# Performance work log

Measured on AMD Instinct MI355X. Metric: run time of the kernel, lower is better.

## Reference

```python
import jax, jax.numpy as jnp
import numpy as np

EPS = 1e-5

def _layer_norm(x, gamma, beta):
    m = jnp.mean(x, axis=-1, keepdims=True)
    v = jnp.mean(jnp.square(x - m), axis=-1, keepdims=True)
    return (x - m) * jax.lax.rsqrt(v + EPS) * gamma + beta

def setup_inputs() -> dict:
    key = jax.random.key(0)
    ks = jax.random.split(key, 6)
    B, D, H = 4096, 1024, 1024
    s = 1.0 / np.sqrt(H)
    return {
        "inputs": jax.random.normal(ks[0], (B, D), jnp.float32),
        "hx": jax.random.normal(ks[1], (B, H), jnp.float32),
        "cx": jax.random.normal(ks[2], (B, H), jnp.float32),
        "w_ih": jax.random.uniform(ks[3], (4 * H, D), jnp.float32, -s, s),
        "w_hh": jax.random.uniform(ks[4], (4 * H, H), jnp.float32, -s, s),
        "b_hh": jax.random.uniform(ks[5], (4 * H,), jnp.float32, -s, s),
        "g_ih": jnp.ones((4 * H,), jnp.float32),
        "beta_ih": jnp.zeros((4 * H,), jnp.float32),
        "g_hh": jnp.ones((4 * H,), jnp.float32),
        "beta_hh": jnp.zeros((4 * H,), jnp.float32),
        "g_ho": jnp.ones((H,), jnp.float32),
        "beta_ho": jnp.zeros((H,), jnp.float32),
    }

def reference(inputs, hx, cx, w_ih, w_hh, b_hh, g_ih, beta_ih, g_hh, beta_hh, g_ho, beta_ho):
    # i2h: [B, 4H] (no input bias used in original forward)
    i2h = inputs @ w_ih.T
    h2h = hx @ w_hh.T + b_hh
    gates = _layer_norm(i2h, g_ih, beta_ih) + _layer_norm(h2h, g_hh, beta_hh)
    i, f, o, g = jnp.split(gates, 4, axis=1)  # torch chunk order: i, f, o, g
    cy = jax.nn.sigmoid(f) * cx + jax.nn.sigmoid(i) * jnp.tanh(g)
    hy = jax.nn.sigmoid(o) * _layer_norm(jnp.tanh(cy), g_ho, beta_ho)
    # Dropout(0.1) is identity in eval / deterministic reference
    return hy, cy
```

## Files before the change

### kernel.cpp

```cpp
#include <hip/hip_runtime.h>
#include <hip/hip_bf16.h>
#include <stdint.h>

typedef __attribute__((ext_vector_type(8))) short bf16x8;
typedef __attribute__((ext_vector_type(4))) float f32x4;

#define LN_EPS 1e-5f

__device__ inline unsigned f2bf(float f) {
    unsigned u = __builtin_bit_cast(unsigned, f);
    u += 0x7fffu + ((u >> 16) & 1u);
    return u >> 16;
}
__device__ inline float bf2f(unsigned u) {
    return __builtin_bit_cast(float, u << 16);
}
__device__ inline float sigf(float x) {
    return 1.0f / (1.0f + __expf(-x));
}
__device__ inline float tanh_fast(float x) {
    return __builtin_fmaf(2.0f, 1.0f / (1.0f + __expf(-2.0f * x)), -1.0f);
}
__device__ inline float wred(float v) {
#pragma unroll
    for (int o = 32; o > 0; o >>= 1) v += __shfl_xor(v, o);
    return v;
}
__device__ inline void gload_lds16(const void* g, void* l) {
    __builtin_amdgcn_global_load_lds(
        (const __attribute__((address_space(1))) void*)g,
        (__attribute__((address_space(3))) void*)l, 16, 0, 0);
}

__global__ __launch_bounds__(256) void cast_all(
    const float4* __restrict__ s0, ushort4* __restrict__ d0, int n0,
    const float4* __restrict__ s1, ushort4* __restrict__ d1, int n1,
    const float4* __restrict__ s2, ushort4* __restrict__ d2, int n2,
    const float4* __restrict__ s3, ushort4* __restrict__ d3, int n3)
{
    int j = blockIdx.x * blockDim.x + threadIdx.x;
    const float4* s; ushort4* d;
    if (j < n0) { s = s0; d = d0; }
    else {
        j -= n0;
        if (j < n1) { s = s1; d = d1; }
        else {
            j -= n1;
            if (j < n2) { s = s2; d = d2; }
            else {
                j -= n2;
                if (j >= n3) return;
                s = s3; d = d3;
            }
        }
    }
    float4 v = s[j];
    ushort4 o;
    o.x = (unsigned short)f2bf(v.x); o.y = (unsigned short)f2bf(v.y);
    o.z = (unsigned short)f2bf(v.z); o.w = (unsigned short)f2bf(v.w);
    d[j] = o;
}

#define GNT 32

__global__ __launch_bounds__(512) void gemm8p(
    const short* __restrict__ Aa, const short* __restrict__ Ba, unsigned short* __restrict__ Ca,
    const short* __restrict__ Ab, const short* __restrict__ Bb, unsigned short* __restrict__ Cb,
    const float* __restrict__ Bias,
    float2* __restrict__ P,
    int N, int K)
{
    __shared__ __attribute__((aligned(16))) short lds[65536];
    short* ldsA = lds;
    short* ldsB = lds + 32768;

    const int gx  = gridDim.x;
    const int gxy = gx * gridDim.y;
    int bid = (blockIdx.z * gridDim.y + blockIdx.y) * gx + blockIdx.x;
    const int cpx = (gxy * gridDim.z) >> 3;
    int swz = (bid & 7) * cpx + (bid >> 3);
    const int z  = swz / gxy;
    const int r2 = swz - z * gxy;
    const int by = r2 / gx;
    const int bx = r2 - by * gx;

    const short* __restrict__ A = z ? Ab : Aa;
    const short* __restrict__ B = z ? Bb : Ba;
    unsigned short* __restrict__ C = z ? Cb : Ca;
    const int brow = by * 256, bcol = bx * 256;

    const int t    = threadIdx.x;
    const int lane = t & 63, w = t >> 6;
    const int wr = w >> 2, wc = w & 3;
    const int lr = lane & 15, kc = lane >> 4;

    const int ci0 = t, ci1 = t + 512;
    const int r0 = ci0 >> 2, l0 = (ci0 & 3) ^ ((r0 >> 1) & 3);
    const int r1 = ci1 >> 2, l1 = (ci1 & 3) ^ ((r1 >> 1) & 3);
    const int gA0 = (brow + r0) * K + l0 * 8;
    const int gA1 = (brow + r1) * K + l1 * 8;
    const int gB0 = (bcol + r0) * K + l0 * 8;
    const int gB1 = (bcol + r1) * K + l1 * 8;
    const int d0 = ci0 * 8, d1 = ci1 * 8;

#define STAGE_A(u) { const int so_ = ((u) & 3) * 8192; \
    gload_lds16(A + gA0 + (u) * 32, ldsA + so_ + d0);  \
    gload_lds16(A + gA1 + (u) * 32, ldsA + so_ + d1); }
#define STAGE_B(u) { const int so_ = ((u) & 3) * 8192; \
    gload_lds16(B + gB0 + (u) * 32, ldsB + so_ + d0);  \
    gload_lds16(B + gB1 + (u) * 32, ldsB + so_ + d1); }

    int offW[8], offX[4];
#pragma unroll
    for (int f = 0; f < 8; ++f) {
        int r = wr * 128 + f * 16 + lr;
        offW[f] = r * 32 + ((kc ^ ((r >> 1) & 3)) * 8);
    }
#pragma unroll
    for (int n = 0; n < 4; ++n) {
        int r = wc * 64 + n * 16 + lr;
        offX[n] = r * 32 + ((kc ^ ((r >> 1) & 3)) * 8);
    }

    f32x4 acc[8][4];
#pragma unroll
    for (int i = 0; i < 8; ++i)
#pragma unroll
        for (int j = 0; j < 4; ++j)
            acc[i][j] = (f32x4){0.f, 0.f, 0.f, 0.f};

    STAGE_A(0); STAGE_B(0); STAGE_A(1); STAGE_B(1); STAGE_A(2);
    asm volatile("s_waitcnt vmcnt(6)" ::: "memory");
    __builtin_amdgcn_s_barrier();

#pragma unroll 4
    for (int T = 0; T < GNT; ++T) {
        const int so = (T & 3) * 8192;
        bf16x8 w0, w1, w2, w3, x0, x1, x2, x3;

        w0 = *(const bf16x8*)&ldsB[so + offW[0]];
        w1 = *(const bf16x8*)&ldsB[so + offW[1]];
        w2 = *(const bf16x8*)&ldsB[so + offW[2]];
        w3 = *(const bf16x8*)&ldsB[so + offW[3]];
        x0 = *(const bf16x8*)&ldsA[so + offX[0]];
        x1 = *(const bf16x8*)&ldsA[so + offX[1]];
        x2 = *(const bf16x8*)&ldsA[so + offX[2]];
        x3 = *(const bf16x8*)&ldsA[so + offX[3]];
        if (T + 2 < GNT) STAGE_B(T + 2);
        __builtin_amdgcn_s_barrier();
        asm volatile("s_waitcnt lgkmcnt(0)" ::: "memory");
        __builtin_amdgcn_sched_barrier(0);
        __builtin_amdgcn_s_setprio(1);
        acc[0][0] = __builtin_amdgcn_mfma_f32_16x16x32_bf16(w0, x0, acc[0][0], 0, 0, 0);
        acc[0][1] = __builtin_amdgcn_mfma_f32_16x16x32_bf16(w0, x1, acc[0][1], 0, 0, 0);
        acc[0][2] = __builtin_amdgcn_mfma_f32_16x16x32_bf16(w0, x2, acc[0][2], 0, 0, 0);
        acc[0][3] = __builtin_amdgcn_mfma_f32_16x16x32_bf16(w0, x3, acc[0][3], 0, 0, 0);
        acc[1][0] = __builtin_amdgcn_mfma_f32_16x16x32_bf16(w1, x0, acc[1][0], 0, 0, 0);
        acc[1][1] = __builtin_amdgcn_mfma_f32_16x16x32_bf16(w1, x1, acc[1][1], 0, 0, 0);
        acc[1][2] = __builtin_amdgcn_mfma_f32_16x16x32_bf16(w1, x2, acc[1][2], 0, 0, 0);
        acc[1][3] = __builtin_amdgcn_mfma_f32_16x16x32_bf16(w1, x3, acc[1][3], 0, 0, 0);
        acc[2][0] = __builtin_amdgcn_mfma_f32_16x16x32_bf16(w2, x0, acc[2][0], 0, 0, 0);
        acc[2][1] = __builtin_amdgcn_mfma_f32_16x16x32_bf16(w2, x1, acc[2][1], 0, 0, 0);
        acc[2][2] = __builtin_amdgcn_mfma_f32_16x16x32_bf16(w2, x2, acc[2][2], 0, 0, 0);
        acc[2][3] = __builtin_amdgcn_mfma_f32_16x16x32_bf16(w2, x3, acc[2][3], 0, 0, 0);
        acc[3][0] = __builtin_amdgcn_mfma_f32_16x16x32_bf16(w3, x0, acc[3][0], 0, 0, 0);
        acc[3][1] = __builtin_amdgcn_mfma_f32_16x16x32_bf16(w3, x1, acc[3][1], 0, 0, 0);
        acc[3][2] = __builtin_amdgcn_mfma_f32_16x16x32_bf16(w3, x2, acc[3][2], 0, 0, 0);
        acc[3][3] = __builtin_amdgcn_mfma_f32_16x16x32_bf16(w3, x3, acc[3][3], 0, 0, 0);
        __builtin_amdgcn_s_setprio(0);
        __builtin_amdgcn_s_barrier();

        w0 = *(const bf16x8*)&ldsB[so + offW[4]];
        w1 = *(const bf16x8*)&ldsB[so + offW[5]];
        w2 = *(const bf16x8*)&ldsB[so + offW[6]];
        w3 = *(const bf16x8*)&ldsB[so + offW[7]];
        if (T + 3 < GNT) STAGE_A(T + 3);
        __builtin_amdgcn_s_barrier();
        asm volatile("s_waitcnt lgkmcnt(0)" ::: "memory");
        __builtin_amdgcn_sched_barrier(0);
        __builtin_amdgcn_s_setprio(1);
        acc[4][0] = __builtin_amdgcn_mfma_f32_16x16x32_bf16(w0, x0, acc[4][0], 0, 0, 0);
        acc[4][1] = __builtin_amdgcn_mfma_f32_16x16x32_bf16(w0, x1, acc[4][1], 0, 0, 0);
        acc[4][2] = __builtin_amdgcn_mfma_f32_16x16x32_bf16(w0, x2, acc[4][2], 0, 0, 0);
        acc[4][3] = __builtin_amdgcn_mfma_f32_16x16x32_bf16(w0, x3, acc[4][3], 0, 0, 0);
        acc[5][0] = __builtin_amdgcn_mfma_f32_16x16x32_bf16(w1, x0, acc[5][0], 0, 0, 0);
        acc[5][1] = __builtin_amdgcn_mfma_f32_16x16x32_bf16(w1, x1, acc[5][1], 0, 0, 0);
        acc[5][2] = __builtin_amdgcn_mfma_f32_16x16x32_bf16(w1, x2, acc[5][2], 0, 0, 0);
        acc[5][3] = __builtin_amdgcn_mfma_f32_16x16x32_bf16(w1, x3, acc[5][3], 0, 0, 0);
        acc[6][0] = __builtin_amdgcn_mfma_f32_16x16x32_bf16(w2, x0, acc[6][0], 0, 0, 0);
        acc[6][1] = __builtin_amdgcn_mfma_f32_16x16x32_bf16(w2, x1, acc[6][1], 0, 0, 0);
        acc[6][2] = __builtin_amdgcn_mfma_f32_16x16x32_bf16(w2, x2, acc[6][2], 0, 0, 0);
        acc[6][3] = __builtin_amdgcn_mfma_f32_16x16x32_bf16(w2, x3, acc[6][3], 0, 0, 0);
        acc[7][0] = __builtin_amdgcn_mfma_f32_16x16x32_bf16(w3, x0, acc[7][0], 0, 0, 0);
        acc[7][1] = __builtin_amdgcn_mfma_f32_16x16x32_bf16(w3, x1, acc[7][1], 0, 0, 0);
        acc[7][2] = __builtin_amdgcn_mfma_f32_16x16x32_bf16(w3, x2, acc[7][2], 0, 0, 0);
        acc[7][3] = __builtin_amdgcn_mfma_f32_16x16x32_bf16(w3, x3, acc[7][3], 0, 0, 0);
        __builtin_amdgcn_s_setprio(0);
        if (T < GNT - 3)      { asm volatile("s_waitcnt vmcnt(6)" ::: "memory"); }
        else if (T == GNT - 3){ asm volatile("s_waitcnt vmcnt(4)" ::: "memory"); }
        else if (T == GNT - 2){ asm volatile("s_waitcnt vmcnt(0)" ::: "memory"); }
        __builtin_amdgcn_s_barrier();
    }

    float4 bias4[8];
#pragma unroll
    for (int f = 0; f < 8; ++f) {
        if (z) bias4[f] = *reinterpret_cast<const float4*>(&Bias[bcol + wr * 128 + f * 16 + kc * 4]);
        else   bias4[f] = (float4){0.f, 0.f, 0.f, 0.f};
    }

    uint2 pk[8][4];
    float s[4] = {0.f, 0.f, 0.f, 0.f}, q[4] = {0.f, 0.f, 0.f, 0.f};
#pragma unroll
    for (int f = 0; f < 8; ++f) {
#pragma unroll
        for (int n = 0; n < 4; ++n) {
            float v0 = acc[f][n][0] + bias4[f].x;
            float v1 = acc[f][n][1] + bias4[f].y;
            float v2 = acc[f][n][2] + bias4[f].z;
            float v3 = acc[f][n][3] + bias4[f].w;
            unsigned u0 = f2bf(v0), u1 = f2bf(v1), u2 = f2bf(v2), u3 = f2bf(v3);
            float e0 = bf2f(u0), e1 = bf2f(u1), e2 = bf2f(u2), e3 = bf2f(u3);
            s[n] += (e0 + e1) + (e2 + e3);
            q[n] += (e0 * e0 + e1 * e1) + (e2 * e2 + e3 * e3);
            pk[f][n].x = u0 | (u1 << 16);
            pk[f][n].y = u2 | (u3 << 16);
        }
    }
#pragma unroll
    for (int n = 0; n < 4; ++n) {
        s[n] += __shfl_xor(s[n], 16); s[n] += __shfl_xor(s[n], 32);
        q[n] += __shfl_xor(q[n], 16); q[n] += __shfl_xor(q[n], 32);
    }

    __syncthreads();
    float2* part = (float2*)lds;
    if (kc == 0) {
#pragma unroll
        for (int n = 0; n < 4; ++n) {
            float2 pr; pr.x = s[n]; pr.y = q[n];
            part[wr * 256 + wc * 64 + n * 16 + lr] = pr;
        }
    }
    __syncthreads();
    if (t < 256) {
        float2 p0 = part[t], p1 = part[256 + t];
        float2 o; o.x = p0.x + p1.x; o.y = p0.y + p1.y;
        P[((size_t)(z * 16 + by) * 256 + t) * 16 + bx] = o;
    }
    __syncthreads();

    uint8_t* cb = (uint8_t*)lds;
    const int rloc0 = wc * 64 + lr;
#pragma unroll
    for (int f = 0; f < 8; ++f) {
        const int colB = wr * 256 + f * 32 + kc * 8;
#pragma unroll
        for (int n = 0; n < 4; ++n) {
            const int r = rloc0 + n * 16;
            *reinterpret_cast<uint2*>(cb + r * 512 + (colB ^ ((r & 7) << 4))) = pk[f][n];
        }
    }
    __syncthreads();
    {
        const int rr = t >> 5;
        const int cB = (t & 31) * 16;
#pragma unroll
        for (int i = 0; i < 16; ++i) {
            const int r = rr + i * 16;
            uint4 v = *reinterpret_cast<const uint4*>(cb + r * 512 + (cB ^ ((r & 7) << 4)));
            *reinterpret_cast<uint4*>((uint8_t*)&C[(size_t)(brow + r) * N + bcol] + cB) = v;
        }
    }
#undef STAGE_A
#undef STAGE_B
}

__global__ __launch_bounds__(256) void ln_lstm(
    const unsigned short* __restrict__ i2h,
    const unsigned short* __restrict__ h2h,
    const float* __restrict__ cx,
    const float2* __restrict__ P,
    const float* __restrict__ g_ih, const float* __restrict__ be_ih,
    const float* __restrict__ g_hh, const float* __restrict__ be_hh,
    const float* __restrict__ g_ho, const float* __restrict__ be_ho,
    float* __restrict__ hy, float* __restrict__ cy, int H, int B)
{
    const int b = blockIdx.x;
    const int t = threadIdx.x;
    const int lane = t & 63;
    const int wave = t >> 6;
    const int H4 = 4 * H;
    const int h0 = t * 4;

    const unsigned short* xi = i2h + (size_t)b * H4;
    const unsigned short* xh = h2h + (size_t)b * H4;

    __shared__ float red[4][2];
    __shared__ float st[4];

    if (wave == 0) {
        const int half = (lane >> 4) & 1;
        float2 v = (float2){0.f, 0.f};
        if (lane < 32) v = P[((size_t)(half * B + b)) * 16 + (lane & 15)];
        v.x += __shfl_xor(v.x, 1); v.y += __shfl_xor(v.y, 1);
        v.x += __shfl_xor(v.x, 2); v.y += __shfl_xor(v.y, 2);
        v.x += __shfl_xor(v.x, 4); v.y += __shfl_xor(v.y, 4);
        v.x += __shfl_xor(v.x, 8); v.y += __shfl_xor(v.y, 8);
        if (lane < 32 && (lane & 15) == 0) {
            const float inv4H = 1.0f / (float)H4;
            float m = v.x * inv4H;
            float r = rsqrtf(v.y * inv4H - m * m + LN_EPS);
            st[half * 2]     = m;
            st[half * 2 + 1] = r;
        }
    }
    __syncthreads();
    const float mI = st[0], rI = st[1], mH = st[2], rH = st[3];

    float gate[4][4];
#pragma unroll
    for (int q = 0; q < 4; ++q) {
        const int j = q * H + h0;
        ushort4 vi = *reinterpret_cast<const ushort4*>(&xi[j]);
        ushort4 vh = *reinterpret_cast<const ushort4*>(&xh[j]);
        float4 gi = *reinterpret_cast<const float4*>(&g_ih[j]);
        float4 bi = *reinterpret_cast<const float4*>(&be_ih[j]);
        float4 gh = *reinterpret_cast<const float4*>(&g_hh[j]);
        float4 bh = *reinterpret_cast<const float4*>(&be_hh[j]);
        gate[q][0] = (bf2f(vi.x) - mI) * rI * gi.x + bi.x + (bf2f(vh.x) - mH) * rH * gh.x + bh.x;
        gate[q][1] = (bf2f(vi.y) - mI) * rI * gi.y + bi.y + (bf2f(vh.y) - mH) * rH * gh.y + bh.y;
        gate[q][2] = (bf2f(vi.z) - mI) * rI * gi.z + bi.z + (bf2f(vh.z) - mH) * rH * gh.z + bh.z;
        gate[q][3] = (bf2f(vi.w) - mI) * rI * gi.w + bi.w + (bf2f(vh.w) - mH) * rH * gh.w + bh.w;
    }

    float4 cxv = *reinterpret_cast<const float4*>(&cx[(size_t)b * H + h0]);
    float cvals[4] = {cxv.x, cxv.y, cxv.z, cxv.w};
    float tv[4], ov[4];
    float s2 = 0.f, q2 = 0.f;
    float4 cyv;
#pragma unroll
    for (int k = 0; k < 4; ++k) {
        float c = sigf(gate[1][k]) * cvals[k] + sigf(gate[0][k]) * tanh_fast(gate[3][k]);
        ((float*)&cyv)[k] = c;
        float tc = tanh_fast(c);
        tv[k] = tc; ov[k] = sigf(gate[2][k]);
        s2 += tc; q2 += tc * tc;
    }
    *reinterpret_cast<float4*>(&cy[(size_t)b * H + h0]) = cyv;

    s2 = wred(s2); q2 = wred(q2);
    if (lane == 0) { red[wave][0] = s2; red[wave][1] = q2; }
    __syncthreads();
    float S2 = red[0][0] + red[1][0] + red[2][0] + red[3][0];
    float Q2 = red[0][1] + red[1][1] + red[2][1] + red[3][1];
    const float invH = 1.0f / (float)H;
    float mt = S2 * invH;
    float rt = rsqrtf(Q2 * invH - mt * mt + LN_EPS);

    float4 go = *reinterpret_cast<const float4*>(&g_ho[h0]);
    float4 bo = *reinterpret_cast<const float4*>(&be_ho[h0]);
    float4 hyv;
    hyv.x = ov[0] * ((tv[0] - mt) * rt * go.x + bo.x);
    hyv.y = ov[1] * ((tv[1] - mt) * rt * go.y + bo.y);
    hyv.z = ov[2] * ((tv[2] - mt) * rt * go.z + bo.z);
    hyv.w = ov[3] * ((tv[3] - mt) * rt * go.w + bo.w);
    *reinterpret_cast<float4*>(&hy[(size_t)b * H + h0]) = hyv;
}

extern "C" void kernel_launch(void* const* d_in, const int* in_sizes, int n_in,
                              void* d_out, int out_size, void* d_ws, size_t ws_size,
                              hipStream_t stream) {
    const float* inputs  = (const float*)d_in[0];
    const float* hx      = (const float*)d_in[1];
    const float* cx      = (const float*)d_in[2];
    const float* w_ih    = (const float*)d_in[3];
    const float* w_hh    = (const float*)d_in[4];
    const float* b_hh    = (const float*)d_in[5];
    const float* g_ih    = (const float*)d_in[6];
    const float* beta_ih = (const float*)d_in[7];
    const float* g_hh    = (const float*)d_in[8];
    const float* beta_hh = (const float*)d_in[9];
    const float* g_ho    = (const float*)d_in[10];
    const float* beta_ho = (const float*)d_in[11];

    const int H  = in_sizes[10];
    const int B  = in_sizes[1] / H;
    const int D  = in_sizes[0] / B;
    const int H4 = 4 * H;

    uint8_t* ws = (uint8_t*)d_ws;
    size_t off = 0;
    short* Abf  = (short*)(ws + off); off += (size_t)B * D * 2;
    short* Hbf  = (short*)(ws + off); off += (size_t)B * H * 2;
    short* Wih  = (short*)(ws + off); off += (size_t)H4 * D * 2;
    short* Whh  = (short*)(ws + off); off += (size_t)H4 * H * 2;
    unsigned short* i2hb = (unsigned short*)(ws + off); off += (size_t)B * H4 * 2;
    unsigned short* h2hb = (unsigned short*)(ws + off); off += (size_t)B * H4 * 2;
    float2* P   = (float2*)(ws + off); off += (size_t)2 * B * 16 * sizeof(float2);

    float* hy  = (float*)d_out;
    float* cyo = (float*)d_out + (size_t)B * H;

    {
        const int n0 = (B * D) / 4, n1 = (B * H) / 4, n2 = (H4 * D) / 4, n3 = (H4 * H) / 4;
        const int tot = n0 + n1 + n2 + n3;
        cast_all<<<(tot + 255) / 256, 256, 0, stream>>>(
            (const float4*)inputs, (ushort4*)Abf, n0,
            (const float4*)hx,     (ushort4*)Hbf, n1,
            (const float4*)w_ih,   (ushort4*)Wih, n2,
            (const float4*)w_hh,   (ushort4*)Whh, n3);
    }

    {
        dim3 grid(H4 / 256, B / 256, 2);
        gemm8p<<<grid, 512, 0, stream>>>(Abf, Wih, i2hb, Hbf, Whh, h2hb, b_hh, P, H4, D);
    }

    ln_lstm<<<B, 256, 0, stream>>>(i2hb, h2hb, cx, P,
                                   g_ih, beta_ih, g_hh, beta_hh, g_ho, beta_ho,
                                   hy, cyo, H, B);
}
```

Baseline: 126.5 us.

## Store GEMM outputs in fragment-native layout and gather in LSTM kernel

The GEMM epilogue no longer stages the bf16 output tile and the row statistics through LDS with several block barriers. Each lane writes its MFMA fragments directly in a fragment-native (tiled) layout, and per-wave partial sums go straight to a wider partials buffer. The LSTM kernel now gathers each row's scattered fragments into shared memory with async global-to-LDS loads, then decodes the permuted indices. This trades epilogue barriers and LDS traffic for a more complex gather and a wider partial reduction in the consumer kernel.

```diff
diff --git a/kernel.cpp b/kernel.cpp
--- a/kernel.cpp
+++ b/kernel.cpp
@@ -68,7 +68,7 @@
     const short* __restrict__ Ab, const short* __restrict__ Bb, unsigned short* __restrict__ Cb,
     const float* __restrict__ Bias,
     float2* __restrict__ P,
-    int N, int K)
+    int N, int K, int Bn)
 {
     __shared__ __attribute__((aligned(16))) short lds[65536];
     short* ldsA = lds;
@@ -202,10 +202,13 @@
         __builtin_amdgcn_s_barrier();
     }
 
+    const int gc0 = bcol + wr * 128 + kc * 4;
+    const int mr0 = brow + wc * 64 + lr;
+
     float4 bias4[8];
 #pragma unroll
     for (int f = 0; f < 8; ++f) {
-        if (z) bias4[f] = *reinterpret_cast<const float4*>(&Bias[bcol + wr * 128 + f * 16 + kc * 4]);
+        if (z) bias4[f] = *reinterpret_cast<const float4*>(&Bias[gc0 + f * 16]);
         else   bias4[f] = (float4){0.f, 0.f, 0.f, 0.f};
     }
 
@@ -232,44 +235,23 @@
         s[n] += __shfl_xor(s[n], 16); s[n] += __shfl_xor(s[n], 32);
         q[n] += __shfl_xor(q[n], 16); q[n] += __shfl_xor(q[n], 32);
     }
-
-    __syncthreads();
-    float2* part = (float2*)lds;
     if (kc == 0) {
 #pragma unroll
         for (int n = 0; n < 4; ++n) {
             float2 pr; pr.x = s[n]; pr.y = q[n];
-            part[wr * 256 + wc * 64 + n * 16 + lr] = pr;
+            P[(size_t)(z * Bn + mr0 + n * 16) * 32 + bx * 2 + wr] = pr;
         }
     }
-    __syncthreads();
-    if (t < 256) {
-        float2 p0 = part[t], p1 = part[256 + t];
-        float2 o; o.x = p0.x + p1.x; o.y = p0.y + p1.y;
-        P[((size_t)(z * 16 + by) * 256 + t) * 16 + bx] = o;
-    }
-    __syncthreads();
-
-    uint8_t* cb = (uint8_t*)lds;
-    const int rloc0 = wc * 64 + lr;
-#pragma unroll
-    for (int f = 0; f < 8; ++f) {
-        const int colB = wr * 256 + f * 32 + kc * 8;
-#pragma unroll
-        for (int n = 0; n < 4; ++n) {
-            const int r = rloc0 + n * 16;
-            *reinterpret_cast<uint2*>(cb + r * 512 + (colB ^ ((r & 7) << 4))) = pk[f][n];
-        }
-    }
-    __syncthreads();
-    {
-        const int rr = t >> 5;
-        const int cB = (t & 31) * 16;
-#pragma unroll
-        for (int i = 0; i < 16; ++i) {
-            const int r = rr + i * 16;
-            uint4 v = *reinterpret_cast<const uint4*>(cb + r * 512 + (cB ^ ((r & 7) << 4)));
-            *reinterpret_cast<uint4*>((uint8_t*)&C[(size_t)(brow + r) * N + bcol] + cB) = v;
+
+#pragma unroll
+    for (int n = 0; n < 4; ++n) {
+#pragma unroll
+        for (int f2 = 0; f2 < 4; ++f2) {
+            uint4 v;
+            v.x = pk[2 * f2][n].x;     v.y = pk[2 * f2][n].y;
+            v.z = pk[2 * f2 + 1][n].x; v.w = pk[2 * f2 + 1][n].y;
+            const size_t uso = ((size_t)((((by * 16 + bx) * 8 + w) * 4 + n) * 4 + f2)) * 512 + lane * 8;
+            *reinterpret_cast<uint4*>(&C[uso]) = v;
         }
     }
 #undef STAGE_A
@@ -277,8 +259,8 @@
 }
 
 __global__ __launch_bounds__(256) void ln_lstm(
-    const unsigned short* __restrict__ i2h,
-    const unsigned short* __restrict__ h2h,
+    const unsigned short* __restrict__ i2hL,
+    const unsigned short* __restrict__ h2hL,
     const float* __restrict__ cx,
     const float2* __restrict__ P,
     const float* __restrict__ g_ih, const float* __restrict__ be_ih,
@@ -291,23 +273,36 @@
     const int lane = t & 63;
     const int wave = t >> 6;
     const int H4 = 4 * H;
-    const int h0 = t * 4;
-
-    const unsigned short* xi = i2h + (size_t)b * H4;
-    const unsigned short* xh = h2h + (size_t)b * H4;
-
+
+    const int by = b >> 8, wc = (b >> 6) & 3, n = (b >> 4) & 3, lr = b & 15;
+
+    __shared__ __attribute__((aligned(16))) unsigned short g8[8192];
     __shared__ float red[4][2];
     __shared__ float st[4];
 
+#pragma unroll
+    for (int k = 0; k < 4; ++k) {
+        const int qp = t + k * 256;
+        const int mt = qp >> 9;
+        const int r  = qp & 511;
+        const int c  = r >> 2;
+        const int f2 = r & 3;
+        const int bxg = c >> 3, wrg = (c >> 2) & 1, kcg = c & 3;
+        const unsigned short* mat = mt ? h2hL : i2hL;
+        const size_t uso = ((size_t)((((by * 16 + bxg) * 8 + (wrg * 4 + wc)) * 4 + n) * 4 + f2)) * 512
+                         + (kcg * 16 + lr) * 8;
+        gload_lds16(mat + uso, g8 + (size_t)qp * 8);
+    }
+
     if (wave == 0) {
-        const int half = (lane >> 4) & 1;
-        float2 v = (float2){0.f, 0.f};
-        if (lane < 32) v = P[((size_t)(half * B + b)) * 16 + (lane & 15)];
-        v.x += __shfl_xor(v.x, 1); v.y += __shfl_xor(v.y, 1);
-        v.x += __shfl_xor(v.x, 2); v.y += __shfl_xor(v.y, 2);
-        v.x += __shfl_xor(v.x, 4); v.y += __shfl_xor(v.y, 4);
-        v.x += __shfl_xor(v.x, 8); v.y += __shfl_xor(v.y, 8);
-        if (lane < 32 && (lane & 15) == 0) {
+        const int half = lane >> 5;
+        float2 v = P[((size_t)half * B + b) * 32 + (lane & 31)];
+        v.x += __shfl_xor(v.x, 1);  v.y += __shfl_xor(v.y, 1);
+        v.x += __shfl_xor(v.x, 2);  v.y += __shfl_xor(v.y, 2);
+        v.x += __shfl_xor(v.x, 4);  v.y += __shfl_xor(v.y, 4);
+        v.x += __shfl_xor(v.x, 8);  v.y += __shfl_xor(v.y, 8);
+        v.x += __shfl_xor(v.x, 16); v.y += __shfl_xor(v.y, 16);
+        if ((lane & 31) == 0) {
             const float inv4H = 1.0f / (float)H4;
             float m = v.x * inv4H;
             float r = rsqrtf(v.y * inv4H - m * m + LN_EPS);
@@ -318,20 +313,29 @@
     __syncthreads();
     const float mI = st[0], rI = st[1], mH = st[2], rH = st[3];
 
+    const int h0 = t * 4;
     float gate[4][4];
 #pragma unroll
-    for (int q = 0; q < 4; ++q) {
-        const int j = q * H + h0;
-        ushort4 vi = *reinterpret_cast<const ushort4*>(&xi[j]);
-        ushort4 vh = *reinterpret_cast<const ushort4*>(&xh[j]);
+    for (int qd = 0; qd < 4; ++qd) {
+        const int g = qd * 1024 + h0;
+        const int c = (g >> 8) * 8 + ((g >> 7) & 1) * 4 + ((g >> 2) & 3);
+        const int f = (g >> 4) & 7;
+        const int widx = (c * 4 + (f >> 1)) * 8 + (f & 1) * 4;
+        uint2 vi2 = *reinterpret_cast<const uint2*>(&g8[widx]);
+        uint2 vh2 = *reinterpret_cast<const uint2*>(&g8[4096 + widx]);
+        const int j = qd * H + h0;
         float4 gi = *reinterpret_cast<const float4*>(&g_ih[j]);
         float4 bi = *reinterpret_cast<const float4*>(&be_ih[j]);
         float4 gh = *reinterpret_cast<const float4*>(&g_hh[j]);
         float4 bh = *reinterpret_cast<const float4*>(&be_hh[j]);
-        gate[q][0] = (bf2f(vi.x) - mI) * rI * gi.x + bi.x + (bf2f(vh.x) - mH) * rH * gh.x + bh.x;
-        gate[q][1] = (bf2f(vi.y) - mI) * rI * gi.y + bi.y + (bf2f(vh.y) - mH) * rH * gh.y + bh.y;
-        gate[q][2] = (bf2f(vi.z) - mI) * rI * gi.z + bi.z + (bf2f(vh.z) - mH) * rH * gh.z + bh.z;
-        gate[q][3] = (bf2f(vi.w) - mI) * rI * gi.w + bi.w + (bf2f(vh.w) - mH) * rH * gh.w + bh.w;
+        float xi0 = bf2f(vi2.x & 0xffffu), xi1 = bf2f(vi2.x >> 16);
+        float xi2 = bf2f(vi2.y & 0xffffu), xi3 = bf2f(vi2.y >> 16);
+        float xh0 = bf2f(vh2.x & 0xffffu), xh1 = bf2f(vh2.x >> 16);
+        float xh2 = bf2f(vh2.y & 0xffffu), xh3 = bf2f(vh2.y >> 16);
+        gate[qd][0] = (xi0 - mI) * rI * gi.x + bi.x + (xh0 - mH) * rH * gh.x + bh.x;
+        gate[qd][1] = (xi1 - mI) * rI * gi.y + bi.y + (xh1 - mH) * rH * gh.y + bh.y;
+        gate[qd][2] = (xi2 - mI) * rI * gi.z + bi.z + (xh2 - mH) * rH * gh.z + bh.z;
+        gate[qd][3] = (xi3 - mI) * rI * gi.w + bi.w + (xh3 - mH) * rH * gh.w + bh.w;
     }
 
     float4 cxv = *reinterpret_cast<const float4*>(&cx[(size_t)b * H + h0]);
@@ -355,16 +359,16 @@
     float S2 = red[0][0] + red[1][0] + red[2][0] + red[3][0];
     float Q2 = red[0][1] + red[1][1] + red[2][1] + red[3][1];
     const float invH = 1.0f / (float)H;
-    float mt = S2 * invH;
-    float rt = rsqrtf(Q2 * invH - mt * mt + LN_EPS);
+    float mt2 = S2 * invH;
+    float rt = rsqrtf(Q2 * invH - mt2 * mt2 + LN_EPS);
 
     float4 go = *reinterpret_cast<const float4*>(&g_ho[h0]);
     float4 bo = *reinterpret_cast<const float4*>(&be_ho[h0]);
     float4 hyv;
-    hyv.x = ov[0] * ((tv[0] - mt) * rt * go.x + bo.x);
-    hyv.y = ov[1] * ((tv[1] - mt) * rt * go.y + bo.y);
-    hyv.z = ov[2] * ((tv[2] - mt) * rt * go.z + bo.z);
-    hyv.w = ov[3] * ((tv[3] - mt) * rt * go.w + bo.w);
+    hyv.x = ov[0] * ((tv[0] - mt2) * rt * go.x + bo.x);
+    hyv.y = ov[1] * ((tv[1] - mt2) * rt * go.y + bo.y);
+    hyv.z = ov[2] * ((tv[2] - mt2) * rt * go.z + bo.z);
+    hyv.w = ov[3] * ((tv[3] - mt2) * rt * go.w + bo.w);
     *reinterpret_cast<float4*>(&hy[(size_t)b * H + h0]) = hyv;
 }
 
@@ -397,7 +401,7 @@
     short* Whh  = (short*)(ws + off); off += (size_t)H4 * H * 2;
     unsigned short* i2hb = (unsigned short*)(ws + off); off += (size_t)B * H4 * 2;
     unsigned short* h2hb = (unsigned short*)(ws + off); off += (size_t)B * H4 * 2;
-    float2* P   = (float2*)(ws + off); off += (size_t)2 * B * 16 * sizeof(float2);
+    float2* P   = (float2*)(ws + off); off += (size_t)2 * B * 32 * sizeof(float2);
 
     float* hy  = (float*)d_out;
     float* cyo = (float*)d_out + (size_t)B * H;
@@ -414,7 +418,7 @@
 
     {
         dim3 grid(H4 / 256, B / 256, 2);
-        gemm8p<<<grid, 512, 0, stream>>>(Abf, Wih, i2hb, Hbf, Whh, h2hb, b_hh, P, H4, D);
+        gemm8p<<<grid, 512, 0, stream>>>(Abf, Wih, i2hb, Hbf, Whh, h2hb, b_hh, P, H4, D, B);
     }
 
     ln_lstm<<<B, 256, 0, stream>>>(i2hb, h2hb, cx, P,
```

Result: slower. 182.8 us (+44.6%).
